# Kernel tuning notes

Measured on AMD Instinct MI355X. Metric: run time of the kernel, lower is better.

Reference implementation:

```python
import jax, jax.numpy as jnp
import numpy as np

DIM_MODEL = 1024
DIM_K = 64
DIM_V = 64
H = 16
B = 2
S = 2048


def setup_inputs() -> dict:
    key = jax.random.key(0)
    ks = jax.random.split(key, 11)
    s = 0.02
    return {
        "Q": jax.random.normal(ks[0], (B, S, DIM_MODEL), jnp.float32),
        "K": jax.random.normal(ks[1], (B, S, DIM_MODEL), jnp.float32),
        "V": jax.random.normal(ks[2], (B, S, DIM_MODEL), jnp.float32),
        "Wq": jax.random.normal(ks[3], (DIM_MODEL, H * DIM_K), jnp.float32) * s,
        "bq": jnp.zeros((H * DIM_K,), jnp.float32),
        "Wk": jax.random.normal(ks[4], (DIM_MODEL, H * DIM_K), jnp.float32) * s,
        "bk": jnp.zeros((H * DIM_K,), jnp.float32),
        "Wv": jax.random.normal(ks[5], (DIM_MODEL, H * DIM_V), jnp.float32) * s,
        "bv": jnp.zeros((H * DIM_V,), jnp.float32),
        "Wo": jax.random.normal(ks[6], (H * DIM_V, DIM_MODEL), jnp.float32) * s,
        "bo": jnp.zeros((DIM_MODEL,), jnp.float32),
    }


def reference(Q, K, V, Wq, bq, Wk, bk, Wv, bv, Wo, bo):
    b, len_q = Q.shape[0], Q.shape[1]
    # QKV projections, split heads: [b, h, S, d]
    q = (Q @ Wq + bq).reshape(b, len_q, H, DIM_K).transpose(0, 2, 1, 3)
    k = (K @ Wk + bk).reshape(b, K.shape[1], H, DIM_K).transpose(0, 2, 1, 3)
    v = (V @ Wv + bv).reshape(b, V.shape[1], H, DIM_V).transpose(0, 2, 1, 3)
    # FAITHFUL QUIRK: original scales by sqrt(K.shape[0]) == batch size, not dim_k
    scale = 1.0 / np.sqrt(b).astype(np.float32)
    att = jnp.einsum('bhqd,bhkd->bhqk', q * scale, k)
    att = jax.nn.softmax(att, axis=-1)
    out = jnp.einsum('bhqk,bhkd->bhqd', att, v)  # [b,h,S,dv]
    out = out.transpose(0, 2, 1, 3).reshape(b, len_q, H * DIM_V)
    return out @ Wo + bo
```

## Files before the change

### kernel.cpp

```cpp
#include <hip/hip_runtime.h>
#include <hip/hip_bf16.h>


using bf16 = __hip_bfloat16;
typedef __attribute__((ext_vector_type(4))) float f32x4;
typedef __attribute__((ext_vector_type(8))) short bf16x8;

__device__ __forceinline__ void gload_lds16(const void* gsrc, void* ldst) {
    __builtin_amdgcn_global_load_lds(
        (const __attribute__((address_space(1))) void*)gsrc,
        (__attribute__((address_space(3))) void*)ldst,
        16, 0, 0);
}

__device__ __forceinline__ float fexp2(float x) {
    float r; asm("v_exp_f32 %0, %1" : "=v"(r) : "v"(x)); return r;
}

__device__ __forceinline__ unsigned cvtpk(float a, float b) {
    unsigned d; asm("v_cvt_pk_bf16_f32 %0, %1, %2" : "=v"(d) : "v"(a), "v"(b));
    return d;
}

__device__ __forceinline__ void pls32(unsigned &a, unsigned &b) {
    asm("v_permlane32_swap_b32 %0, %1" : "+v"(a), "+v"(b));
}
__device__ __forceinline__ void pls16(unsigned &a, unsigned &b) {
    asm("v_permlane16_swap_b32 %0, %1" : "+v"(a), "+v"(b));
}

__device__ __forceinline__ unsigned pack2bf(float a, float b) {
    unsigned short ua = __builtin_bit_cast(unsigned short, __float2bfloat16(a));
    unsigned short ub = __builtin_bit_cast(unsigned short, __float2bfloat16(b));
    return (unsigned)ua | ((unsigned)ub << 16);
}

__global__ void transpose4_kernel(const float* __restrict__ W0, const float* __restrict__ W1,
                                  const float* __restrict__ W2, const float* __restrict__ W3,
                                  bf16* __restrict__ T0, bf16* __restrict__ T1,
                                  bf16* __restrict__ T2, bf16* __restrict__ T3) {
    int z = blockIdx.z;
    const float* W = z == 0 ? W0 : (z == 1 ? W1 : (z == 2 ? W2 : W3));
    bf16* WT = z == 0 ? T0 : (z == 1 ? T1 : (z == 2 ? T2 : T3));
    __shared__ float t[32][33];
    int bx = blockIdx.x * 32, by = blockIdx.y * 32;
    int x = threadIdx.x, y = threadIdx.y;
    #pragma unroll
    for (int i = 0; i < 4; ++i)
        t[y + 8*i][x] = W[(size_t)(by + y + 8*i) * 1024 + bx + x];
    __syncthreads();
    #pragma unroll
    for (int i = 0; i < 4; ++i)
        WT[(size_t)(bx + y + 8*i) * 1024 + by + x] = __float2bfloat16(t[x][y + 8*i]);
}

template<bool AF32>
__global__ __launch_bounds__(256, 3)
void gemm_bt(const void* __restrict__ A0, const void* __restrict__ A1, const void* __restrict__ A2,
             const bf16* __restrict__ B0, const bf16* __restrict__ B1, const bf16* __restrict__ B2,
             const float* __restrict__ bi0, const float* __restrict__ bi1, const float* __restrict__ bi2,
             void* __restrict__ O0, void* __restrict__ O1, void* __restrict__ O2,
             int mode_base)
{
    const int f = blockIdx.x;
    const int s = f >> 3;
    const int y = s & 7;
    const int t = (f & 7) + 8 * (s >> 3);
    const int x = t & 31, z = t >> 5;
    const void* Av = z == 0 ? A0 : (z == 1 ? A1 : A2);
    const bf16* BT = z == 0 ? B0 : (z == 1 ? B1 : B2);
    const float* bias = z == 0 ? bi0 : (z == 1 ? bi1 : bi2);
    void* Cout = z == 0 ? O0 : (z == 1 ? O1 : O2);
    const int mode = mode_base + z;

    __shared__ __align__(16) char Abuf[AF32 ? 32768 : 16384];
    __shared__ __align__(16) char Bbuf[16384];
    const int tid = threadIdx.x;
    const int wave = tid >> 6, lane = tid & 63;
    const int g = lane >> 4, ln = lane & 15;
    const int m0 = x * 128, n0 = y * 128;
    const int wm = (wave >> 1) * 64, wn = (wave & 1) * 64;

    f32x4 acc[4][4] = {};

    for (int k0 = 0; k0 < 1024; k0 += 64) {
        __syncthreads();
        #pragma unroll
        for (int rd = 0; rd < 4; ++rd) {
            int row = rd * 32 + (tid >> 3);
            int src = ((tid & 7) * 16) ^ (((tid >> 3) & 7) << 4);
            gload_lds16((const char*)(BT + (size_t)(n0 + row) * 1024 + k0) + src,
                        Bbuf + rd * 4096 + tid * 16);
        }
        if (AF32) {
            #pragma unroll
            for (int rd = 0; rd < 8; ++rd) {
                int row = rd * 16 + (tid >> 4);
                int src = ((tid & 15) * 16) ^ (((tid >> 4) & 7) << 4);
                gload_lds16((const char*)((const float*)Av + (size_t)(m0 + row) * 1024 + k0) + src,
                            Abuf + rd * 4096 + tid * 16);
            }
        } else {
            #pragma unroll
            for (int rd = 0; rd < 4; ++rd) {
                int row = rd * 32 + (tid >> 3);
                int src = ((tid & 7) * 16) ^ (((tid >> 3) & 7) << 4);
                gload_lds16((const char*)((const bf16*)Av + (size_t)(m0 + row) * 1024 + k0) + src,
                            Abuf + rd * 4096 + tid * 16);
            }
        }
        __syncthreads();
        #pragma unroll
        for (int kk = 0; kk < 2; ++kk) {
            bf16x8 af[4], bfr[4];
            #pragma unroll
            for (int mf = 0; mf < 4; ++mf) {
                int row = wm + mf * 16 + ln;
                if (AF32) {
                    int c0 = kk * 128 + g * 32;
                    int sw = (row & 7) << 4;
                    f32x4 v0 = *(const f32x4*)(Abuf + row * 256 + (c0 ^ sw));
                    f32x4 v1 = *(const f32x4*)(Abuf + row * 256 + ((c0 + 16) ^ sw));
                    union { unsigned u[4]; bf16x8 v; } afu;
                    afu.u[0] = cvtpk(v0[0], v0[1]); afu.u[1] = cvtpk(v0[2], v0[3]);
                    afu.u[2] = cvtpk(v1[0], v1[1]); afu.u[3] = cvtpk(v1[2], v1[3]);
                    af[mf] = afu.v;
                } else {
                    af[mf] = *(const bf16x8*)(Abuf + row * 128 + ((kk*64 + g*16) ^ ((row & 7) << 4)));
                }
            }
            #pragma unroll
            for (int nf = 0; nf < 4; ++nf) {
                int row = wn + nf * 16 + ln;
                bfr[nf] = *(const bf16x8*)(Bbuf + row * 128 + ((kk*64 + g*16) ^ ((row & 7) << 4)));
            }
            #pragma unroll
            for (int mf = 0; mf < 4; ++mf)
                #pragma unroll
                for (int nf = 0; nf < 4; ++nf)
                    acc[mf][nf] = __builtin_amdgcn_mfma_f32_16x16x32_bf16(af[mf], bfr[nf], acc[mf][nf], 0, 0, 0);
        }
    }

    const float scl = (mode == 0) ? (0.70710678118654752f * 1.44269504088896340f) : 1.0f;
    #pragma unroll
    for (int mf = 0; mf < 4; ++mf) {
        #pragma unroll
        for (int nf = 0; nf < 4; ++nf) {
            int col = n0 + wn + nf*16 + ln;
            float bv = bias[col];
            #pragma unroll
            for (int r = 0; r < 4; ++r) {
                int row = m0 + wm + mf*16 + g*4 + r;
                float v = (acc[mf][nf][r] + bv) * scl;
                if (mode == 0 || mode == 1) {
                    ((bf16*)Cout)[(size_t)row * 1024 + col] = __float2bfloat16(v);
                } else if (mode == 2) {
                    int b = row >> 11, ss = row & 2047;
                    int hh = col >> 6, dv = col & 63;
                    ((bf16*)Cout)[(((size_t)(b*16 + hh) * 64 + dv) << 11) + ss] = __float2bfloat16(v);
                } else {
                    ((float*)Cout)[(size_t)row * 1024 + col] = v;
                }
            }
        }
    }
}

__global__ __launch_bounds__(256, 2)
void attn_kernel(const bf16* __restrict__ qh, const bf16* __restrict__ kh,
                 const bf16* __restrict__ vt, bf16* __restrict__ aout)
{
    __shared__ __align__(16) bf16 Kls[2][64 * 64];
    __shared__ __align__(16) bf16 Vls[2][64 * 64];
    const int f = blockIdx.x;
    const int xcd = f & 7, s = f >> 3, i = s & 15, ghi = s >> 4;
    const int bh = xcd + 8 * ghi;
    const int b = bh >> 4, h = bh & 15;
    const int q0 = i * 128;

    const int tid = threadIdx.x;
    const int wave = tid >> 6, lane = tid & 63;
    const int g = lane >> 4, ln = lane & 15;
    const int srow = lane >> 3;
    const int scol = ((lane & 7) * 16) ^ ((srow & 7) << 4);
    const int lnsw = (ln & 7) << 4;

    const bf16* kbase = kh + (size_t)(b * 2048) * 1024 + h * 64;
    const bf16* vbase = vt + (size_t)bh * 64 * 2048;

    bf16x8 qf[2][2];
    #pragma unroll
    for (int nf = 0; nf < 2; ++nf) {
        const bf16* qrow = qh + (size_t)(b*2048 + q0 + wave*32 + nf*16 + ln) * 1024 + h*64;
        qf[nf][0] = *(const bf16x8*)(qrow + g*8);
        qf[nf][1] = *(const bf16x8*)(qrow + 32 + g*8);
    }

    #pragma unroll
    for (int c2 = 0; c2 < 2; ++c2) {
        int c = wave * 2 + c2;
        int row = c * 8 + srow;
        gload_lds16((const char*)(kbase + (size_t)row * 1024) + scol, (char*)&Kls[0][0] + c * 1024);
        gload_lds16((const char*)(vbase + (size_t)row * 2048) + scol, (char*)&Vls[0][0] + c * 1024);
    }

    f32x4 oacc[4][2] = {};
    float lsum[2] = {0.f, 0.f};
    union PU { unsigned u[4]; bf16x8 v; };

    for (int t = 0; t < 32; ++t) {
        const int cur = t & 1;
        if (t < 31) {
            const int kv0n = (t + 1) * 64;
            #pragma unroll
            for (int c2 = 0; c2 < 2; ++c2) {
                int c = wave * 2 + c2;
                int row = c * 8 + srow;
                gload_lds16((const char*)(kbase + (size_t)(kv0n + row) * 1024) + scol,
                            (char*)&Kls[cur ^ 1][0] + c * 1024);
                gload_lds16((const char*)(vbase + (size_t)row * 2048 + kv0n) + scol,
                            (char*)&Vls[cur ^ 1][0] + c * 1024);
            }
            asm volatile("s_waitcnt vmcnt(4)\n\ts_barrier" ::: "memory");
        } else {
            asm volatile("s_waitcnt vmcnt(0)\n\ts_barrier" ::: "memory");
        }
        __builtin_amdgcn_sched_barrier(0);

        const char* Kc = (const char*)&Kls[cur][0];
        const char* Vc = (const char*)&Vls[cur][0];

        f32x4 sac[4][2] = {};
        __builtin_amdgcn_s_setprio(1);
        #pragma unroll
        for (int kk = 0; kk < 2; ++kk) {
            bf16x8 kf[4];
            #pragma unroll
            for (int mf = 0; mf < 4; ++mf)
                kf[mf] = *(const bf16x8*)(Kc + (mf*16 + ln) * 128 + ((kk*64 + g*16) ^ lnsw));
            #pragma unroll
            for (int mf = 0; mf < 4; ++mf)
                #pragma unroll
                for (int nf = 0; nf < 2; ++nf)
                    sac[mf][nf] = __builtin_amdgcn_mfma_f32_16x16x32_bf16(kf[mf], qf[nf][kk], sac[mf][nf], 0, 0, 0);
        }
        __builtin_amdgcn_s_setprio(0);

        PU pf[2][2];
        #pragma unroll
        for (int nf = 0; nf < 2; ++nf) {
            unsigned w[4][2];
            #pragma unroll
            for (int mf = 0; mf < 4; ++mf) {
                float e0 = fexp2(sac[mf][nf][0]);
                float e1 = fexp2(sac[mf][nf][1]);
                float e2 = fexp2(sac[mf][nf][2]);
                float e3 = fexp2(sac[mf][nf][3]);
                lsum[nf] += (e0 + e1) + (e2 + e3);
                w[mf][0] = cvtpk(e0, e1);
                w[mf][1] = cvtpk(e2, e3);
            }
            #pragma unroll
            for (int kk = 0; kk < 2; ++kk) {
                #pragma unroll
                for (int rp = 0; rp < 2; ++rp) {
                    unsigned a = w[2*kk][rp], bb = w[2*kk + 1][rp];
                    pls32(a, bb);
                    pls16(a, bb);
                    pf[nf][kk].u[rp] = a;
                    pf[nf][kk].u[2 + rp] = bb;
                }
            }
        }

        __builtin_amdgcn_s_setprio(1);
        #pragma unroll
        for (int kk = 0; kk < 2; ++kk) {
            bf16x8 vf[4];
            #pragma unroll
            for (int mf = 0; mf < 4; ++mf)
                vf[mf] = *(const bf16x8*)(Vc + (mf*16 + ln) * 128 + ((kk*64 + g*16) ^ lnsw));
            #pragma unroll
            for (int mf = 0; mf < 4; ++mf)
                #pragma unroll
                for (int nf = 0; nf < 2; ++nf)
                    oacc[mf][nf] = __builtin_amdgcn_mfma_f32_16x16x32_bf16(vf[mf], pf[nf][kk].v, oacc[mf][nf], 0, 0, 0);
        }
        __builtin_amdgcn_s_setprio(0);
        __builtin_amdgcn_sched_barrier(0);
        asm volatile("s_barrier" ::: "memory");
    }

    #pragma unroll
    for (int nf = 0; nf < 2; ++nf) {
        float l = lsum[nf];
        l += __shfl_xor(l, 16);
        l += __shfl_xor(l, 32);
        float inv = 1.0f / l;
        int q = q0 + wave*32 + nf*16 + ln;
        bf16* orow = aout + (size_t)(b*2048 + q) * 1024 + h * 64;
        #pragma unroll
        for (int mf = 0; mf < 4; ++mf) {
            *(uint2*)(orow + mf*16 + g*4) = make_uint2(
                pack2bf(oacc[mf][nf][0] * inv, oacc[mf][nf][1] * inv),
                pack2bf(oacc[mf][nf][2] * inv, oacc[mf][nf][3] * inv));
        }
    }
}

extern "C" void kernel_launch(void* const* d_in, const int* in_sizes, int n_in,
                              void* d_out, int out_size, void* d_ws, size_t ws_size,
                              hipStream_t stream)
{
    const float* Q  = (const float*)d_in[0];
    const float* K  = (const float*)d_in[1];
    const float* V  = (const float*)d_in[2];
    const float* Wq = (const float*)d_in[3];
    const float* bq = (const float*)d_in[4];
    const float* Wk = (const float*)d_in[5];
    const float* bk = (const float*)d_in[6];
    const float* Wv = (const float*)d_in[7];
    const float* bv = (const float*)d_in[8];
    const float* Wo = (const float*)d_in[9];
    const float* bo = (const float*)d_in[10];

    char* ws = (char*)d_ws;
    const size_t MB = 1024 * 1024;
    bf16* WqT  = (bf16*)(ws + 24*MB);
    bf16* WkT  = (bf16*)(ws + 26*MB);
    bf16* WvT  = (bf16*)(ws + 28*MB);
    bf16* WoT  = (bf16*)(ws + 30*MB);
    bf16* qhp  = (bf16*)(ws + 32*MB);
    bf16* khp  = (bf16*)(ws + 40*MB);
    bf16* vtp  = (bf16*)(ws + 48*MB);
    bf16* aout = (bf16*)(ws + 0);

    transpose4_kernel<<<dim3(32, 32, 4), dim3(32, 8), 0, stream>>>(Wq, Wk, Wv, Wo, WqT, WkT, WvT, WoT);

    gemm_bt<true><<<768, 256, 0, stream>>>(Q, K, V, WqT, WkT, WvT,
                                           bq, bk, bv, qhp, khp, vtp, 0);

    attn_kernel<<<512, 256, 0, stream>>>(qhp, khp, vtp, aout);

    gemm_bt<false><<<256, 256, 0, stream>>>(aout, aout, aout, WoT, WoT, WoT,
                                            bo, bo, bo, d_out, d_out, d_out, 3);
}
```

Baseline: 124.3 us.

## Double-buffer GEMM LDS tiles and convert fp32 A to bf16 before LDS

```diff
diff --git a/kernel.cpp b/kernel.cpp
--- a/kernel.cpp
+++ b/kernel.cpp
@@ -55,7 +55,7 @@
 }
 
 template<bool AF32>
-__global__ __launch_bounds__(256, 3)
+__global__ __launch_bounds__(256, 2)
 void gemm_bt(const void* __restrict__ A0, const void* __restrict__ A1, const void* __restrict__ A2,
              const bf16* __restrict__ B0, const bf16* __restrict__ B1, const bf16* __restrict__ B2,
              const float* __restrict__ bi0, const float* __restrict__ bi1, const float* __restrict__ bi2,
@@ -73,72 +73,92 @@
     void* Cout = z == 0 ? O0 : (z == 1 ? O1 : O2);
     const int mode = mode_base + z;
 
-    __shared__ __align__(16) char Abuf[AF32 ? 32768 : 16384];
-    __shared__ __align__(16) char Bbuf[16384];
+    __shared__ __align__(16) char Abuf[2][16384];
+    __shared__ __align__(16) char Bbuf[2][16384];
     const int tid = threadIdx.x;
     const int wave = tid >> 6, lane = tid & 63;
     const int g = lane >> 4, ln = lane & 15;
     const int m0 = x * 128, n0 = y * 128;
     const int wm = (wave >> 1) * 64, wn = (wave & 1) * 64;
+    const int lnsw = (ln & 7) << 4;
 
     f32x4 acc[4][4] = {};
-
-    for (int k0 = 0; k0 < 1024; k0 += 64) {
-        __syncthreads();
+    f32x4 areg[8];
+
+    const int arow0 = wave * 32 + (lane >> 4);
+    const int acol = (lane & 15) * 4;
+    const int awr = (lane & 15) * 8;
+
+    auto loadA = [&](int k0, int bufsel) {
+        if (AF32) {
+            #pragma unroll
+            for (int j = 0; j < 8; ++j) {
+                int row = arow0 + j * 4;
+                areg[j] = *(const f32x4*)((const float*)Av + (size_t)(m0 + row) * 1024 + k0 + acol);
+            }
+        } else {
+            #pragma unroll
+            for (int rd = 0; rd < 4; ++rd) {
+                int row = rd * 32 + (tid >> 3);
+                int src = ((tid & 7) * 16) ^ (((tid >> 3) & 7) << 4);
+                gload_lds16((const char*)((const bf16*)Av + (size_t)(m0 + row) * 1024 + k0) + src,
+                            &Abuf[bufsel][rd * 4096 + tid * 16]);
+            }
+        }
+    };
+    auto writeA = [&](int bufsel) {
+        if (AF32) {
+            #pragma unroll
+            for (int j = 0; j < 8; ++j) {
+                int row = arow0 + j * 4;
+                *(uint2*)&Abuf[bufsel][row * 128 + (awr ^ ((row & 7) << 4))] =
+                    make_uint2(cvtpk(areg[j][0], areg[j][1]), cvtpk(areg[j][2], areg[j][3]));
+            }
+        }
+    };
+    auto stageB = [&](int k0, int bufsel) {
         #pragma unroll
         for (int rd = 0; rd < 4; ++rd) {
             int row = rd * 32 + (tid >> 3);
             int src = ((tid & 7) * 16) ^ (((tid >> 3) & 7) << 4);
             gload_lds16((const char*)(BT + (size_t)(n0 + row) * 1024 + k0) + src,
-                        Bbuf + rd * 4096 + tid * 16);
-        }
-        if (AF32) {
-            #pragma unroll
-            for (int rd = 0; rd < 8; ++rd) {
-                int row = rd * 16 + (tid >> 4);
-                int src = ((tid & 15) * 16) ^ (((tid >> 4) & 7) << 4);
-                gload_lds16((const char*)((const float*)Av + (size_t)(m0 + row) * 1024 + k0) + src,
-                            Abuf + rd * 4096 + tid * 16);
-            }
-        } else {
-            #pragma unroll
-            for (int rd = 0; rd < 4; ++rd) {
-                int row = rd * 32 + (tid >> 3);
-                int src = ((tid & 7) * 16) ^ (((tid >> 3) & 7) << 4);
-                gload_lds16((const char*)((const bf16*)Av + (size_t)(m0 + row) * 1024 + k0) + src,
-                            Abuf + rd * 4096 + tid * 16);
-            }
-        }
-        __syncthreads();
+                        &Bbuf[bufsel][rd * 4096 + tid * 16]);
+        }
+    };
+
+    loadA(0, 0);
+    stageB(0, 0);
+    writeA(0);
+    asm volatile("s_waitcnt vmcnt(0) lgkmcnt(0)\n\ts_barrier" ::: "memory");
+
+    for (int k = 0; k < 16; ++k) {
+        const int cur = k & 1;
+        if (k < 15) {
+            loadA((k + 1) * 64, cur ^ 1);
+            stageB((k + 1) * 64, cur ^ 1);
+        }
+        __builtin_amdgcn_sched_barrier(0);
+        __builtin_amdgcn_s_setprio(1);
         #pragma unroll
         for (int kk = 0; kk < 2; ++kk) {
             bf16x8 af[4], bfr[4];
             #pragma unroll
-            for (int mf = 0; mf < 4; ++mf) {
-                int row = wm + mf * 16 + ln;
-                if (AF32) {
-                    int c0 = kk * 128 + g * 32;
-                    int sw = (row & 7) << 4;
-                    f32x4 v0 = *(const f32x4*)(Abuf + row * 256 + (c0 ^ sw));
-                    f32x4 v1 = *(const f32x4*)(Abuf + row * 256 + ((c0 + 16) ^ sw));
-                    union { unsigned u[4]; bf16x8 v; } afu;
-                    afu.u[0] = cvtpk(v0[0], v0[1]); afu.u[1] = cvtpk(v0[2], v0[3]);
-                    afu.u[2] = cvtpk(v1[0], v1[1]); afu.u[3] = cvtpk(v1[2], v1[3]);
-                    af[mf] = afu.v;
-                } else {
-                    af[mf] = *(const bf16x8*)(Abuf + row * 128 + ((kk*64 + g*16) ^ ((row & 7) << 4)));
-                }
-            }
-            #pragma unroll
-            for (int nf = 0; nf < 4; ++nf) {
-                int row = wn + nf * 16 + ln;
-                bfr[nf] = *(const bf16x8*)(Bbuf + row * 128 + ((kk*64 + g*16) ^ ((row & 7) << 4)));
-            }
+            for (int mf = 0; mf < 4; ++mf)
+                af[mf] = *(const bf16x8*)&Abuf[cur][(wm + mf*16 + ln) * 128 + ((kk*64 + g*16) ^ lnsw)];
+            #pragma unroll
+            for (int nf = 0; nf < 4; ++nf)
+                bfr[nf] = *(const bf16x8*)&Bbuf[cur][(wn + nf*16 + ln) * 128 + ((kk*64 + g*16) ^ lnsw)];
             #pragma unroll
             for (int mf = 0; mf < 4; ++mf)
                 #pragma unroll
                 for (int nf = 0; nf < 4; ++nf)
                     acc[mf][nf] = __builtin_amdgcn_mfma_f32_16x16x32_bf16(af[mf], bfr[nf], acc[mf][nf], 0, 0, 0);
+        }
+        __builtin_amdgcn_s_setprio(0);
+        __builtin_amdgcn_sched_barrier(0);
+        if (k < 15) {
+            writeA(cur ^ 1);
+            asm volatile("s_waitcnt vmcnt(0) lgkmcnt(0)\n\ts_barrier" ::: "memory");
         }
     }
 
```

Result: slower. 135.4 us (+9.0%).

## Pre-convert activations to bf16 and use narrower N tile for output GEMM

Applied to the files above, without the earlier changes.

```diff
diff --git a/kernel.cpp b/kernel.cpp
--- a/kernel.cpp
+++ b/kernel.cpp
@@ -33,6 +33,21 @@
     unsigned short ua = __builtin_bit_cast(unsigned short, __float2bfloat16(a));
     unsigned short ub = __builtin_bit_cast(unsigned short, __float2bfloat16(b));
     return (unsigned)ua | ((unsigned)ub << 16);
+}
+
+__global__ void conv3_kernel(const float* __restrict__ X0, const float* __restrict__ X1,
+                             const float* __restrict__ X2,
+                             bf16* __restrict__ O0, bf16* __restrict__ O1, bf16* __restrict__ O2,
+                             int n4) {
+    int z = blockIdx.z;
+    const float* in = z == 0 ? X0 : (z == 1 ? X1 : X2);
+    bf16* out = z == 0 ? O0 : (z == 1 ? O1 : O2);
+    int idx = blockIdx.x * blockDim.x + threadIdx.x;
+    int stride = gridDim.x * blockDim.x;
+    for (int i = idx; i < n4; i += stride) {
+        float4 v = reinterpret_cast<const float4*>(in)[i];
+        reinterpret_cast<uint2*>(out)[i] = make_uint2(pack2bf(v.x, v.y), pack2bf(v.z, v.w));
+    }
 }
 
 __global__ void transpose4_kernel(const float* __restrict__ W0, const float* __restrict__ W1,
@@ -54,88 +69,74 @@
         WT[(size_t)(bx + y + 8*i) * 1024 + by + x] = __float2bfloat16(t[x][y + 8*i]);
 }
 
-template<bool AF32>
+template<int NTILE>
 __global__ __launch_bounds__(256, 3)
-void gemm_bt(const void* __restrict__ A0, const void* __restrict__ A1, const void* __restrict__ A2,
+void gemm_bt(const bf16* __restrict__ A0, const bf16* __restrict__ A1, const bf16* __restrict__ A2,
              const bf16* __restrict__ B0, const bf16* __restrict__ B1, const bf16* __restrict__ B2,
              const float* __restrict__ bi0, const float* __restrict__ bi1, const float* __restrict__ bi2,
              void* __restrict__ O0, void* __restrict__ O1, void* __restrict__ O2,
              int mode_base)
 {
     const int f = blockIdx.x;
-    const int s = f >> 3;
-    const int y = s & 7;
-    const int t = (f & 7) + 8 * (s >> 3);
-    const int x = t & 31, z = t >> 5;
-    const void* Av = z == 0 ? A0 : (z == 1 ? A1 : A2);
+    int x, y, z;
+    if (NTILE == 128) {
+        const int s = f >> 3;
+        y = s & 7;
+        const int t = (f & 7) + 8 * (s >> 3);
+        x = t & 31; z = t >> 5;
+    } else {
+        const int s = f >> 3;
+        y = s & 15;
+        x = (f & 7) + 8 * (s >> 4);
+        z = 0;
+    }
+    const bf16* A  = z == 0 ? A0 : (z == 1 ? A1 : A2);
     const bf16* BT = z == 0 ? B0 : (z == 1 ? B1 : B2);
     const float* bias = z == 0 ? bi0 : (z == 1 ? bi1 : bi2);
     void* Cout = z == 0 ? O0 : (z == 1 ? O1 : O2);
     const int mode = mode_base + z;
 
-    __shared__ __align__(16) char Abuf[AF32 ? 32768 : 16384];
-    __shared__ __align__(16) char Bbuf[16384];
+    constexpr int MF = (NTILE == 128) ? 4 : 2;
+    __shared__ __align__(16) char Abuf[16384];
+    __shared__ __align__(16) char Bbuf[NTILE * 128];
     const int tid = threadIdx.x;
     const int wave = tid >> 6, lane = tid & 63;
     const int g = lane >> 4, ln = lane & 15;
-    const int m0 = x * 128, n0 = y * 128;
-    const int wm = (wave >> 1) * 64, wn = (wave & 1) * 64;
-
-    f32x4 acc[4][4] = {};
+    const int m0 = x * 128, n0 = y * NTILE;
+    const int wm = (NTILE == 128) ? (wave >> 1) * 64 : wave * 32;
+    const int wn = (NTILE == 128) ? (wave & 1) * 64 : 0;
+    const int lnsw = (ln & 7) << 4;
+
+    f32x4 acc[MF][4] = {};
 
     for (int k0 = 0; k0 < 1024; k0 += 64) {
         __syncthreads();
         #pragma unroll
         for (int rd = 0; rd < 4; ++rd) {
+            int row = rd * 32 + (tid >> 3);
+            int src = ((tid & 7) * 16) ^ (((tid >> 3) & 7) << 4);
+            gload_lds16((const char*)(A + (size_t)(m0 + row) * 1024 + k0) + src,
+                        Abuf + rd * 4096 + tid * 16);
+        }
+        #pragma unroll
+        for (int rd = 0; rd < NTILE / 32; ++rd) {
             int row = rd * 32 + (tid >> 3);
             int src = ((tid & 7) * 16) ^ (((tid >> 3) & 7) << 4);
             gload_lds16((const char*)(BT + (size_t)(n0 + row) * 1024 + k0) + src,
                         Bbuf + rd * 4096 + tid * 16);
         }
-        if (AF32) {
-            #pragma unroll
-            for (int rd = 0; rd < 8; ++rd) {
-                int row = rd * 16 + (tid >> 4);
-                int src = ((tid & 15) * 16) ^ (((tid >> 4) & 7) << 4);
-                gload_lds16((const char*)((const float*)Av + (size_t)(m0 + row) * 1024 + k0) + src,
-                            Abuf + rd * 4096 + tid * 16);
-            }
-        } else {
-            #pragma unroll
-            for (int rd = 0; rd < 4; ++rd) {
-                int row = rd * 32 + (tid >> 3);
-                int src = ((tid & 7) * 16) ^ (((tid >> 3) & 7) << 4);
-                gload_lds16((const char*)((const bf16*)Av + (size_t)(m0 + row) * 1024 + k0) + src,
-                            Abuf + rd * 4096 + tid * 16);
-            }
-        }
         __syncthreads();
         #pragma unroll
         for (int kk = 0; kk < 2; ++kk) {
-            bf16x8 af[4], bfr[4];
-            #pragma unroll
-            for (int mf = 0; mf < 4; ++mf) {
-                int row = wm + mf * 16 + ln;
-                if (AF32) {
-                    int c0 = kk * 128 + g * 32;
-                    int sw = (row & 7) << 4;
-                    f32x4 v0 = *(const f32x4*)(Abuf + row * 256 + (c0 ^ sw));
-                    f32x4 v1 = *(const f32x4*)(Abuf + row * 256 + ((c0 + 16) ^ sw));
-                    union { unsigned u[4]; bf16x8 v; } afu;
-                    afu.u[0] = cvtpk(v0[0], v0[1]); afu.u[1] = cvtpk(v0[2], v0[3]);
-                    afu.u[2] = cvtpk(v1[0], v1[1]); afu.u[3] = cvtpk(v1[2], v1[3]);
-                    af[mf] = afu.v;
-                } else {
-                    af[mf] = *(const bf16x8*)(Abuf + row * 128 + ((kk*64 + g*16) ^ ((row & 7) << 4)));
-                }
-            }
-            #pragma unroll
-            for (int nf = 0; nf < 4; ++nf) {
-                int row = wn + nf * 16 + ln;
-                bfr[nf] = *(const bf16x8*)(Bbuf + row * 128 + ((kk*64 + g*16) ^ ((row & 7) << 4)));
-            }
-            #pragma unroll
-            for (int mf = 0; mf < 4; ++mf)
+            bf16x8 af[MF], bfr[4];
+            #pragma unroll
+            for (int mf = 0; mf < MF; ++mf)
+                af[mf] = *(const bf16x8*)&Abuf[(wm + mf*16 + ln) * 128 + ((kk*64 + g*16) ^ lnsw)];
+            #pragma unroll
+            for (int nf = 0; nf < 4; ++nf)
+                bfr[nf] = *(const bf16x8*)&Bbuf[(wn + nf*16 + ln) * 128 + ((kk*64 + g*16) ^ lnsw)];
+            #pragma unroll
+            for (int mf = 0; mf < MF; ++mf)
                 #pragma unroll
                 for (int nf = 0; nf < 4; ++nf)
                     acc[mf][nf] = __builtin_amdgcn_mfma_f32_16x16x32_bf16(af[mf], bfr[nf], acc[mf][nf], 0, 0, 0);
@@ -144,7 +145,7 @@
 
     const float scl = (mode == 0) ? (0.70710678118654752f * 1.44269504088896340f) : 1.0f;
     #pragma unroll
-    for (int mf = 0; mf < 4; ++mf) {
+    for (int mf = 0; mf < MF; ++mf) {
         #pragma unroll
         for (int nf = 0; nf < 4; ++nf) {
             int col = n0 + wn + nf*16 + ln;
@@ -327,6 +328,9 @@
 
     char* ws = (char*)d_ws;
     const size_t MB = 1024 * 1024;
+    bf16* Qbf  = (bf16*)(ws + 0);
+    bf16* Kbf  = (bf16*)(ws + 8*MB);
+    bf16* Vbf  = (bf16*)(ws + 16*MB);
     bf16* WqT  = (bf16*)(ws + 24*MB);
     bf16* WkT  = (bf16*)(ws + 26*MB);
     bf16* WvT  = (bf16*)(ws + 28*MB);
@@ -336,13 +340,16 @@
     bf16* vtp  = (bf16*)(ws + 48*MB);
     bf16* aout = (bf16*)(ws + 0);
 
+    const int n4 = (2 * 2048 * 1024) / 4;
+    conv3_kernel<<<dim3(512, 1, 3), 256, 0, stream>>>(Q, K, V, Qbf, Kbf, Vbf, n4);
+
     transpose4_kernel<<<dim3(32, 32, 4), dim3(32, 8), 0, stream>>>(Wq, Wk, Wv, Wo, WqT, WkT, WvT, WoT);
 
-    gemm_bt<true><<<768, 256, 0, stream>>>(Q, K, V, WqT, WkT, WvT,
-                                           bq, bk, bv, qhp, khp, vtp, 0);
+    gemm_bt<128><<<768, 256, 0, stream>>>(Qbf, Kbf, Vbf, WqT, WkT, WvT,
+                                          bq, bk, bv, qhp, khp, vtp, 0);
 
     attn_kernel<<<512, 256, 0, stream>>>(qhp, khp, vtp, aout);
 
-    gemm_bt<false><<<256, 256, 0, stream>>>(aout, aout, aout, WoT, WoT, WoT,
-                                            bo, bo, bo, d_out, d_out, d_out, 3);
-}
+    gemm_bt<64><<<512, 256, 0, stream>>>(aout, aout, aout, WoT, WoT, WoT,
+                                         bo, bo, bo, d_out, d_out, d_out, 3);
+}
```

Result: faster. 119.8 us (-3.6%).
